# Kernel optimization log

Measured on AMD Instinct MI355X. Metric: run time of the kernel, lower is better.

Reference implementation:

```python
import jax, jax.numpy as jnp
import numpy as np

B, S, ENC, DEC, ATT = 32, 2048, 1024, 1024, 1024


def setup_inputs() -> dict:
    key = jax.random.key(0)
    k1, k2, k3, k4, k5 = jax.random.split(key, 5)
    return {
        "keys": jax.random.normal(k1, (B, S, ENC), dtype=jnp.float32),
        "q": jax.random.normal(k2, (B, DEC), dtype=jnp.float32),
        "W_e2a": jax.random.normal(k3, (ATT, ENC), dtype=jnp.float32),
        "W_d2a": jax.random.normal(k4, (ATT, DEC), dtype=jnp.float32),
        "v_w": jax.random.normal(k5, (ATT, 1), dtype=jnp.float32),
    }


def reference(keys, q, W_e2a, W_d2a, v_w):
    # U: [B, S, ATT] = keys @ W_e2a.T
    U = jnp.einsum("bse,ae->bsa", keys, W_e2a)
    # V: [B, ATT] broadcast over S
    V = jnp.einsum("bd,ad->ba", q, W_d2a)
    # scores e: [B, S]
    e = jnp.einsum("bsa,a->bs", jnp.tanh(U + V[:, None, :]), v_w[:, 0])
    a = jax.nn.softmax(e, axis=1)
    # context: [B, ENC]
    context = jnp.einsum("bs,bse->be", a, keys)
    return context
```

## Files before the change

kernel.cpp:

```cpp
#include <hip/hip_runtime.h>
#include <stdint.h>

#define NB 32
#define NS 2048
#define NE 1024
#define ND 1024
#define NA 1024
#define MROWS (NB * NS)

typedef float f32x4 __attribute__((ext_vector_type(4)));
typedef int i32x4 __attribute__((ext_vector_type(4)));

typedef __attribute__((address_space(3))) unsigned int lds_u32;
typedef __attribute__((address_space(1))) unsigned int glb_u32;

__device__ __forceinline__ float tanh_fast(float x){
  float ax = fabsf(x);
  float e = __expf(-2.0f * ax);
  float t = (1.0f - e) * __builtin_amdgcn_rcpf(1.0f + e);
  return x < 0.0f ? -t : t;
}
__device__ __forceinline__ void gload_lds16(const void* g, void* l){
  __builtin_amdgcn_global_load_lds((const glb_u32*)g, (lds_u32*)l, 16, 0, 0);
}

#define BARRIER() asm volatile("s_barrier" ::: "memory")
#define VMCNT0()  asm volatile("s_waitcnt vmcnt(0)" ::: "memory")

__global__ __launch_bounds__(256) void quant_kernel(
    const float* __restrict__ src, unsigned char* __restrict__ dh,
    unsigned char* __restrict__ dl, float* __restrict__ sdst)
{
  const int t = threadIdx.x;
  const int w = t >> 6, l = t & 63;
  const int row = blockIdx.x * 4 + w;
  const float* sp = src + (size_t)row * 1024;

  f32x4 x[4];
  #pragma unroll
  for (int c = 0; c < 4; ++c)
    x[c] = *reinterpret_cast<const f32x4*>(sp + c * 256 + l * 4);

  float m = 0.0f;
  #pragma unroll
  for (int c = 0; c < 4; ++c)
    #pragma unroll
    for (int j = 0; j < 4; ++j) m = fmaxf(m, fabsf(x[c][j]));
  #pragma unroll
  for (int off = 1; off < 64; off <<= 1) m = fmaxf(m, __shfl_xor(m, off, 64));
  m = fmaxf(m, 1e-30f);
  const float s = m * (1.0f / 126.0f);
  const float inv = 126.0f / m;

  const int r = row & 255;
  const int rp = r >> 1, cc = r & 1;
  const int kb = (l >> 2) & 3;
  const int gran = (cc << 2) | (kb ^ (rp & 3));
  const size_t base = ((size_t)(row >> 8) << 18) + ((size_t)rp << 7)
                    + ((size_t)gran << 4) + ((l & 3) << 2);

  #pragma unroll
  for (int c = 0; c < 4; ++c){
    int hw = 0, lw = 0;
    #pragma unroll
    for (int j = 0; j < 4; ++j){
      float f = x[c][j] * inv;
      float hf = rintf(f);
      float lf = fminf(rintf((f - hf) * 256.0f), 127.0f);
      hw |= (((int)hf) & 255) << (8 * j);
      lw |= (((int)lf) & 255) << (8 * j);
    }
    const int g = c * 4 + (l >> 4);
    *reinterpret_cast<int*>(dh + base + ((size_t)g << 14)) = hw;
    *reinterpret_cast<int*>(dl + base + ((size_t)g << 14)) = lw;
  }
  if (l == 0) sdst[row] = s;
}

__global__ __launch_bounds__(256) void v_kernel(
    const float* __restrict__ q, const float* __restrict__ Wd,
    float* __restrict__ V)
{
  int gw = blockIdx.x * 4 + (threadIdx.x >> 6);
  int l = threadIdx.x & 63;
  int b = gw >> 10, a = gw & 1023;
  const float* qp = q + b * ND;
  const float* wp = Wd + (size_t)a * ND;
  float s = 0.0f;
  #pragma unroll
  for (int c = 0; c < 4; ++c){
    int off = c * 256 + l * 4;
    f32x4 q4 = *reinterpret_cast<const f32x4*>(qp + off);
    f32x4 w4 = *reinterpret_cast<const f32x4*>(wp + off);
    s += q4[0]*w4[0] + q4[1]*w4[1] + q4[2]*w4[2] + q4[3]*w4[3];
  }
  #pragma unroll
  for (int off = 1; off < 64; off <<= 1) s += __shfl_xor(s, off, 64);
  if (l == 0) V[gw] = s;
}

__global__ __launch_bounds__(256, 2) void score_i8_kernel(
    const unsigned char* __restrict__ Kq_h,
    const unsigned char* __restrict__ Kq_l,
    const unsigned char* __restrict__ Wq_h,
    const unsigned char* __restrict__ Wq_l,
    const float* __restrict__ sA, const float* __restrict__ sB,
    const float* __restrict__ Vb, const float* __restrict__ vw,
    float* __restrict__ e_part)
{
  __shared__ __align__(16) unsigned char shb[65536];
  __shared__ float ebuf[2][128];
  __shared__ float sAl[128];
  __shared__ float sBl[128];

  const int t = threadIdx.x;
  const int w = t >> 6, l = t & 63;
  const int l15 = l & 15, lg = l >> 4;
  const int wr = w >> 1, wc = w & 1;

  const int orig = blockIdx.x;
  const int xcd = orig & 7;
  const int s0 = orig >> 3;
  const int nchunk = s0 & 7;
  const int mtile = ((s0 >> 3) << 3) | xcd;
  const int row0 = mtile << 7;
  const int nb0 = nchunk << 7;
  const int bb = row0 >> 11;

  const size_t aoff_src = ((size_t)(mtile >> 1) << 18) + ((size_t)(mtile & 1) << 13);
  const unsigned char* Asrc_h = Kq_h + aoff_src;
  const unsigned char* Asrc_l = Kq_l + aoff_src;
  const size_t boff_src = ((size_t)(nchunk >> 1) << 18) + ((size_t)(nchunk & 1) << 13);
  const unsigned char* Bsrc_h = Wq_h + boff_src;
  const unsigned char* Bsrc_l = Wq_l + boff_src;

  const int swz0 = ((l15 & 1) << 2) | (lg ^ ((l15 >> 1) & 3));
  const int aoff0 = (wr << 12) + ((l15 >> 1) << 7) + (swz0 << 4);
  const int boff0 = (wc << 12) + ((l15 >> 1) << 7) + (swz0 << 4);
  const int stoff = t << 4;

  i32x4 acc1[4][4], acc2[4][4];
  #pragma unroll
  for (int mf = 0; mf < 4; ++mf)
    #pragma unroll
    for (int nf = 0; nf < 4; ++nf){ acc1[mf][nf] = (i32x4)0; acc2[mf][nf] = (i32x4)0; }

  auto stage = [&](int g, int bufW){
    const size_t gb = (size_t)g << 14;
    unsigned char* d = shb + bufW;
    gload_lds16(Asrc_h + gb + stoff,        d + stoff);
    gload_lds16(Asrc_h + gb + 4096 + stoff, d + 4096 + stoff);
    gload_lds16(Asrc_l + gb + stoff,        d + 8192 + stoff);
    gload_lds16(Asrc_l + gb + 4096 + stoff, d + 12288 + stoff);
    gload_lds16(Bsrc_h + gb + stoff,        d + 16384 + stoff);
    gload_lds16(Bsrc_h + gb + 4096 + stoff, d + 20480 + stoff);
    gload_lds16(Bsrc_l + gb + stoff,        d + 24576 + stoff);
    gload_lds16(Bsrc_l + gb + 4096 + stoff, d + 28672 + stoff);
  };

  stage(0, 0);
  if (t < 128){ sAl[t] = sA[row0 + t]; sBl[t] = sB[nb0 + t]; }
  __syncthreads();

  #pragma unroll 1
  for (int g = 0; g < 16; ++g){
    const int bufR = (g & 1) * 32768;
    const int bufW = 32768 - bufR;
    if (g < 15) stage(g + 1, bufW);

    const unsigned char* base = shb + bufR;

    i32x4 Ah[4], Bh[4];
    #pragma unroll
    for (int mf = 0; mf < 4; ++mf)
      Ah[mf] = *reinterpret_cast<const i32x4*>(base + aoff0 + mf * 1024);
    #pragma unroll
    for (int nf = 0; nf < 4; ++nf)
      Bh[nf] = *reinterpret_cast<const i32x4*>(base + 16384 + boff0 + nf * 1024);
    __builtin_amdgcn_s_setprio(1);
    #pragma unroll
    for (int nf = 0; nf < 4; ++nf)
      #pragma unroll
      for (int mf = 0; mf < 4; ++mf)
        acc1[mf][nf] = __builtin_amdgcn_mfma_i32_16x16x64_i8(Ah[mf], Bh[nf], acc1[mf][nf], 0, 0, 0);
    __builtin_amdgcn_s_setprio(0);

    i32x4 Al[4];
    #pragma unroll
    for (int mf = 0; mf < 4; ++mf)
      Al[mf] = *reinterpret_cast<const i32x4*>(base + 8192 + aoff0 + mf * 1024);
    __builtin_amdgcn_s_setprio(1);
    #pragma unroll
    for (int nf = 0; nf < 4; ++nf)
      #pragma unroll
      for (int mf = 0; mf < 4; ++mf)
        acc2[mf][nf] = __builtin_amdgcn_mfma_i32_16x16x64_i8(Al[mf], Bh[nf], acc2[mf][nf], 0, 0, 0);
    __builtin_amdgcn_s_setprio(0);

    i32x4 Bl[4];
    #pragma unroll
    for (int nf = 0; nf < 4; ++nf)
      Bl[nf] = *reinterpret_cast<const i32x4*>(base + 24576 + boff0 + nf * 1024);
    __builtin_amdgcn_s_setprio(1);
    #pragma unroll
    for (int nf = 0; nf < 4; ++nf)
      #pragma unroll
      for (int mf = 0; mf < 4; ++mf)
        acc2[mf][nf] = __builtin_amdgcn_mfma_i32_16x16x64_i8(Ah[mf], Bl[nf], acc2[mf][nf], 0, 0, 0);
    __builtin_amdgcn_s_setprio(0);

    VMCNT0();
    BARRIER();
  }

  float sav[16];
  #pragma unroll
  for (int mf = 0; mf < 4; ++mf)
    #pragma unroll
    for (int i = 0; i < 4; ++i)
      sav[(mf << 2) + i] = sAl[(wr << 6) + (mf << 4) + (lg << 2) + i];

  float er[16];
  #pragma unroll
  for (int j = 0; j < 16; ++j) er[j] = 0.0f;
  #pragma unroll
  for (int nf = 0; nf < 4; ++nf){
    const int nl = (wc << 6) + (nf << 4) + l15;
    const int n = nb0 + nl;
    const float sb = sBl[nl];
    const float Vl = Vb[bb * NA + n];
    const float vwl = vw[n];
    #pragma unroll
    for (int mf = 0; mf < 4; ++mf)
      #pragma unroll
      for (int i = 0; i < 4; ++i){
        float U = sav[(mf << 2) + i] * sb *
                  ((float)acc1[mf][nf][i] + (float)acc2[mf][nf][i] * 0.00390625f);
        er[(mf << 2) + i] += tanh_fast(U + Vl) * vwl;
      }
  }
  #pragma unroll
  for (int j = 0; j < 16; ++j){
    #pragma unroll
    for (int off = 1; off < 16; off <<= 1)
      er[j] += __shfl_xor(er[j], off, 64);
  }
  if (l15 == 0){
    #pragma unroll
    for (int mf = 0; mf < 4; ++mf)
      #pragma unroll
      for (int i = 0; i < 4; ++i)
        ebuf[wc][(wr << 6) + (mf << 4) + (lg << 2) + i] = er[(mf << 2) + i];
  }
  __syncthreads();
  if (t < 128)
    e_part[(size_t)nchunk * MROWS + row0 + t] = ebuf[0][t] + ebuf[1][t];
}

__global__ __launch_bounds__(256) void softmax_kernel(
    const float* __restrict__ e_part, float* __restrict__ a)
{
  __shared__ float red[4];
  const int b = blockIdx.x;
  const int t = threadIdx.x;
  const int l = t & 63, w = t >> 6;
  const float* ep = e_part + b * NS + t * 8;
  float v[8];
  #pragma unroll
  for (int j = 0; j < 8; ++j) v[j] = 0.0f;
  #pragma unroll
  for (int c = 0; c < 8; ++c){
    f32x4 x0 = *reinterpret_cast<const f32x4*>(ep + (size_t)c * MROWS);
    f32x4 x1 = *reinterpret_cast<const f32x4*>(ep + (size_t)c * MROWS + 4);
    #pragma unroll
    for (int j = 0; j < 4; ++j){ v[j] += x0[j]; v[4 + j] += x1[j]; }
  }

  float m = v[0];
  #pragma unroll
  for (int j = 1; j < 8; ++j) m = fmaxf(m, v[j]);
  #pragma unroll
  for (int off = 1; off < 64; off <<= 1) m = fmaxf(m, __shfl_xor(m, off, 64));
  if (l == 0) red[w] = m;
  __syncthreads();
  m = fmaxf(fmaxf(red[0], red[1]), fmaxf(red[2], red[3]));
  __syncthreads();

  float ex[8];
  float ssum = 0.0f;
  #pragma unroll
  for (int j = 0; j < 8; ++j){ ex[j] = __expf(v[j] - m); ssum += ex[j]; }
  #pragma unroll
  for (int off = 1; off < 64; off <<= 1) ssum += __shfl_xor(ssum, off, 64);
  if (l == 0) red[w] = ssum;
  __syncthreads();
  ssum = red[0] + red[1] + red[2] + red[3];
  float inv = 1.0f / ssum;

  float o[8];
  #pragma unroll
  for (int j = 0; j < 8; ++j) o[j] = ex[j] * inv;
  float* ap = a + b * NS + t * 8;
  *reinterpret_cast<f32x4*>(ap)     = *reinterpret_cast<f32x4*>(&o[0]);
  *reinterpret_cast<f32x4*>(ap + 4) = *reinterpret_cast<f32x4*>(&o[4]);
}

__global__ __launch_bounds__(256) void ctx_partial_i8_kernel(
    const float* __restrict__ a, const unsigned char* __restrict__ Kq_h,
    const unsigned char* __restrict__ Kq_l, const float* __restrict__ sA,
    float* __restrict__ part)
{
  const int bid = blockIdx.x;
  const int t = threadIdx.x;
  const int g = t >> 4;
  const int kb = (t >> 2) & 3;
  const size_t ibase = ((size_t)bid << 18) + ((size_t)g << 14) + ((size_t)(t & 3) << 2);
  const float* ap = a + bid * 256;
  const float* sp = sA + bid * 256;
  f32x4 accv = (f32x4)0.0f;
  for (int si = 0; si < 256; ++si){
    const int rp = si >> 1, cc = si & 1;
    const size_t addr = ibase + ((size_t)rp << 7)
                      + ((size_t)(((cc << 2) | (kb ^ (rp & 3))) << 4));
    const int h32 = *reinterpret_cast<const int*>(Kq_h + addr);
    const int l32 = *reinterpret_cast<const int*>(Kq_l + addr);
    const float sa = sp[si];
    const float t1 = ap[si] * sa;
    const float t2 = t1 * 0.00390625f;
    #pragma unroll
    for (int j = 0; j < 4; ++j){
      int hj = (h32 << ((3 - j) * 8)) >> 24;
      int lj = (l32 << ((3 - j) * 8)) >> 24;
      accv[j] += t1 * (float)hj + t2 * (float)lj;
    }
  }
  *reinterpret_cast<f32x4*>(part + (size_t)bid * NE + t * 4) = accv;
}

__global__ __launch_bounds__(256) void ctx_reduce_kernel(
    const float* __restrict__ part, float* __restrict__ out)
{
  const int b = blockIdx.x;
  const int t = threadIdx.x;
  f32x4 s = (f32x4)0.0f;
  #pragma unroll
  for (int sc = 0; sc < 8; ++sc)
    s += *reinterpret_cast<const f32x4*>(part + (size_t)((b << 3) + sc) * NE + t * 4);
  *reinterpret_cast<f32x4*>(out + b * NE + t * 4) = s;
}

extern "C" void kernel_launch(void* const* d_in, const int* in_sizes, int n_in,
                              void* d_out, int out_size, void* d_ws, size_t ws_size,
                              hipStream_t stream)
{
  const float* keys = (const float*)d_in[0];
  const float* q    = (const float*)d_in[1];
  const float* We   = (const float*)d_in[2];
  const float* Wd   = (const float*)d_in[3];
  const float* vw   = (const float*)d_in[4];
  float* out = (float*)d_out;

  char* ws = (char*)d_ws;
  const size_t MB = 1024 * 1024;
  unsigned char* Wq_h = (unsigned char*)(ws);
  unsigned char* Wq_l = (unsigned char*)(ws + 1 * MB);
  float* sB     = (float*)(ws + 2 * MB);
  float* sA     = (float*)(ws + 2 * MB + 65536);
  float* Vb     = (float*)(ws + 2 * MB + 393216);
  float* e_part = (float*)(ws + 4 * MB);
  float* a      = (float*)(ws + 6 * MB);
  unsigned char* Kq_h = (unsigned char*)(ws + 8 * MB);
  unsigned char* Kq_l = (unsigned char*)(ws + 72 * MB);
  float* part   = e_part;

  quant_kernel<<<256,   256, 0, stream>>>(We,   Wq_h, Wq_l, sB);
  quant_kernel<<<16384, 256, 0, stream>>>(keys, Kq_h, Kq_l, sA);
  v_kernel<<<(NB * NA) / 4, 256, 0, stream>>>(q, Wd, Vb);
  score_i8_kernel<<<4096, 256, 0, stream>>>(Kq_h, Kq_l, Wq_h, Wq_l,
                                            sA, sB, Vb, vw, e_part);
  softmax_kernel<<<NB, 256, 0, stream>>>(e_part, a);
  ctx_partial_i8_kernel<<<NB * 8, 256, 0, stream>>>(a, Kq_h, Kq_l, sA, part);
  ctx_reduce_kernel<<<NB, 256, 0, stream>>>(part, out);
}
```

Baseline: 330.6 us.

## Load W operand fragments directly from global into registers, halve LDS staging

The B-operand (quantized W hi/lo) tiles are no longer staged through LDS; each wave loads its pre-swizzled fragments directly from global memory into registers, with the hi part register double-buffered one iteration ahead. LDS usage drops from 64KB to 32KB, which could raise occupancy and cuts LDS traffic. In exchange each wave issues uncoalesced-ish 16B global loads for B that are duplicated across waves sharing the same columns, and the loop is manually unrolled by two to ping-pong register buffers, raising register pressure.

```diff
diff --git a/kernel.cpp b/kernel.cpp
--- a/kernel.cpp
+++ b/kernel.cpp
@@ -108,7 +108,7 @@
     const float* __restrict__ Vb, const float* __restrict__ vw,
     float* __restrict__ e_part)
 {
-  __shared__ __align__(16) unsigned char shb[65536];
+  __shared__ __align__(16) unsigned char shb[32768];
   __shared__ float ebuf[2][128];
   __shared__ float sAl[128];
   __shared__ float sBl[128];
@@ -131,58 +131,67 @@
   const unsigned char* Asrc_h = Kq_h + aoff_src;
   const unsigned char* Asrc_l = Kq_l + aoff_src;
   const size_t boff_src = ((size_t)(nchunk >> 1) << 18) + ((size_t)(nchunk & 1) << 13);
-  const unsigned char* Bsrc_h = Wq_h + boff_src;
-  const unsigned char* Bsrc_l = Wq_l + boff_src;
 
   const int swz0 = ((l15 & 1) << 2) | (lg ^ ((l15 >> 1) & 3));
   const int aoff0 = (wr << 12) + ((l15 >> 1) << 7) + (swz0 << 4);
   const int boff0 = (wc << 12) + ((l15 >> 1) << 7) + (swz0 << 4);
   const int stoff = t << 4;
 
+  const unsigned char* pBh = Wq_h + boff_src + boff0;
+  const unsigned char* pBl = Wq_l + boff_src + boff0;
+
   i32x4 acc1[4][4], acc2[4][4];
   #pragma unroll
   for (int mf = 0; mf < 4; ++mf)
     #pragma unroll
     for (int nf = 0; nf < 4; ++nf){ acc1[mf][nf] = (i32x4)0; acc2[mf][nf] = (i32x4)0; }
 
-  auto stage = [&](int g, int bufW){
+  auto stageA = [&](int g, int bufW){
     const size_t gb = (size_t)g << 14;
     unsigned char* d = shb + bufW;
     gload_lds16(Asrc_h + gb + stoff,        d + stoff);
     gload_lds16(Asrc_h + gb + 4096 + stoff, d + 4096 + stoff);
     gload_lds16(Asrc_l + gb + stoff,        d + 8192 + stoff);
     gload_lds16(Asrc_l + gb + 4096 + stoff, d + 12288 + stoff);
-    gload_lds16(Bsrc_h + gb + stoff,        d + 16384 + stoff);
-    gload_lds16(Bsrc_h + gb + 4096 + stoff, d + 20480 + stoff);
-    gload_lds16(Bsrc_l + gb + stoff,        d + 24576 + stoff);
-    gload_lds16(Bsrc_l + gb + 4096 + stoff, d + 28672 + stoff);
   };
 
-  stage(0, 0);
+  i32x4 BhA[4], BhB[4];
+
+  #pragma unroll
+  for (int nf = 0; nf < 4; ++nf)
+    BhA[nf] = *reinterpret_cast<const i32x4*>(pBh + nf * 1024);
+  stageA(0, 0);
   if (t < 128){ sAl[t] = sA[row0 + t]; sBl[t] = sB[nb0 + t]; }
-  __syncthreads();
-
-  #pragma unroll 1
-  for (int g = 0; g < 16; ++g){
-    const int bufR = (g & 1) * 32768;
-    const int bufW = 32768 - bufR;
-    if (g < 15) stage(g + 1, bufW);
-
+  VMCNT0();
+  __syncthreads();
+
+  auto body = [&](int g, i32x4 (&Bhcur)[4], i32x4 (&Bhnext)[4]){
+    const int bufR = (g & 1) << 14;
     const unsigned char* base = shb + bufR;
-
-    i32x4 Ah[4], Bh[4];
+    const size_t gb = (size_t)g << 14;
+
+    if (g < 15){
+      const size_t gb1 = (size_t)(g + 1) << 14;
+      #pragma unroll
+      for (int nf = 0; nf < 4; ++nf)
+        Bhnext[nf] = *reinterpret_cast<const i32x4*>(pBh + gb1 + nf * 1024);
+    }
+    i32x4 Bl[4];
+    #pragma unroll
+    for (int nf = 0; nf < 4; ++nf)
+      Bl[nf] = *reinterpret_cast<const i32x4*>(pBl + gb + nf * 1024);
+    if (g < 15) stageA(g + 1, 16384 - bufR);
+
+    i32x4 Ah[4];
     #pragma unroll
     for (int mf = 0; mf < 4; ++mf)
       Ah[mf] = *reinterpret_cast<const i32x4*>(base + aoff0 + mf * 1024);
+    __builtin_amdgcn_s_setprio(1);
     #pragma unroll
     for (int nf = 0; nf < 4; ++nf)
-      Bh[nf] = *reinterpret_cast<const i32x4*>(base + 16384 + boff0 + nf * 1024);
-    __builtin_amdgcn_s_setprio(1);
-    #pragma unroll
-    for (int nf = 0; nf < 4; ++nf)
       #pragma unroll
       for (int mf = 0; mf < 4; ++mf)
-        acc1[mf][nf] = __builtin_amdgcn_mfma_i32_16x16x64_i8(Ah[mf], Bh[nf], acc1[mf][nf], 0, 0, 0);
+        acc1[mf][nf] = __builtin_amdgcn_mfma_i32_16x16x64_i8(Ah[mf], Bhcur[nf], acc1[mf][nf], 0, 0, 0);
     __builtin_amdgcn_s_setprio(0);
 
     i32x4 Al[4];
@@ -194,13 +203,9 @@
     for (int nf = 0; nf < 4; ++nf)
       #pragma unroll
       for (int mf = 0; mf < 4; ++mf)
-        acc2[mf][nf] = __builtin_amdgcn_mfma_i32_16x16x64_i8(Al[mf], Bh[nf], acc2[mf][nf], 0, 0, 0);
+        acc2[mf][nf] = __builtin_amdgcn_mfma_i32_16x16x64_i8(Al[mf], Bhcur[nf], acc2[mf][nf], 0, 0, 0);
     __builtin_amdgcn_s_setprio(0);
 
-    i32x4 Bl[4];
-    #pragma unroll
-    for (int nf = 0; nf < 4; ++nf)
-      Bl[nf] = *reinterpret_cast<const i32x4*>(base + 24576 + boff0 + nf * 1024);
     __builtin_amdgcn_s_setprio(1);
     #pragma unroll
     for (int nf = 0; nf < 4; ++nf)
@@ -211,6 +216,12 @@
 
     VMCNT0();
     BARRIER();
+  };
+
+  #pragma unroll 1
+  for (int gp = 0; gp < 8; ++gp){
+    body(2 * gp,     BhA, BhB);
+    body(2 * gp + 1, BhB, BhA);
   }
 
   float sav[16];
```

After: 326.2 us. Within noise of the previous version (-1.3%).
